# Kernel optimization log

Hardware: AMD Instinct MI355X
Metric: run time of the kernel (lower is better)

Reference implementation:

```python
import jax, jax.numpy as jnp
import numpy as np

HIDDEN = 4096
N_HEADS = 32
N_KV = 8
HEAD_DIM = 128
ROPE_THETA = 10000.0
B, S = 2, 2048


def _rope_neox(x, cos, sin):
    # x: [B,S,H,D]; cos/sin: [B,S,1,D/2]
    half = x.shape[-1] // 2
    x1, x2 = x[..., :half], x[..., half:]
    return jnp.concatenate([x1 * cos - x2 * sin, x2 * cos + x1 * sin], axis=-1)


def setup_inputs() -> dict:
    key = jax.random.key(0)
    k1, k2, k3 = jax.random.split(key, 3)
    hidden_states = jax.random.normal(k1, (B, S, HIDDEN), dtype=jnp.float32)
    positions = jnp.arange(B * S, dtype=jnp.int32).reshape(B, S)
    q_size = N_HEADS * HEAD_DIM
    kv_size = N_KV * HEAD_DIM
    w_qkv = jax.random.normal(k2, (HIDDEN, q_size + 2 * kv_size), dtype=jnp.float32) * (HIDDEN ** -0.5)
    w_o = jax.random.normal(k3, (q_size, HIDDEN), dtype=jnp.float32) * (q_size ** -0.5)
    return {"hidden_states": hidden_states, "positions": positions, "w_qkv": w_qkv, "w_o": w_o}


def reference(hidden_states, positions, w_qkv, w_o):
    q_size = N_HEADS * HEAD_DIM
    kv_size = N_KV * HEAD_DIM
    b, s, _ = hidden_states.shape

    qkv = hidden_states @ w_qkv  # [B,S,q+2kv]
    q = qkv[..., :q_size].reshape(b, s, N_HEADS, HEAD_DIM)
    k = qkv[..., q_size:q_size + kv_size].reshape(b, s, N_KV, HEAD_DIM)
    v = qkv[..., q_size + kv_size:].reshape(b, s, N_KV, HEAD_DIM)

    # RoPE (neox style, full rotary dim)
    inv_freq = 1.0 / (ROPE_THETA ** (jnp.arange(0, HEAD_DIM, 2, dtype=jnp.float32) / HEAD_DIM))
    ang = positions.astype(jnp.float32)[..., None] * inv_freq  # [B,S,D/2]
    cos = jnp.cos(ang)[:, :, None, :]
    sin = jnp.sin(ang)[:, :, None, :]
    q = _rope_neox(q, cos, sin)
    k = _rope_neox(k, cos, sin)

    # GQA: expand kv heads to match q heads
    rep = N_HEADS // N_KV
    k = jnp.repeat(k, rep, axis=2)  # [B,S,H,D]
    v = jnp.repeat(v, rep, axis=2)

    scale = HEAD_DIM ** -0.5
    scores = jnp.einsum('bqhd,bkhd->bhqk', q, k) * scale  # [B,H,S,S]
    causal = jnp.tril(jnp.ones((s, s), dtype=bool))
    scores = jnp.where(causal[None, None], scores, jnp.finfo(scores.dtype).min)
    probs = jax.nn.softmax(scores, axis=-1)
    attn = jnp.einsum('bhqk,bkhd->bqhd', probs, v).reshape(b, s, q_size)
    return attn @ w_o
```

## Files before the change

### kernel.cpp

```cpp
#include <hip/hip_runtime.h>
#include <hip/hip_bf16.h>
#include <stdint.h>
#include <stddef.h>

typedef unsigned short u16;
typedef __bf16 bf16x8 __attribute__((ext_vector_type(8)));
typedef float f32x4 __attribute__((ext_vector_type(4)));
typedef float f32x16 __attribute__((ext_vector_type(16)));
typedef unsigned u32x2 __attribute__((ext_vector_type(2)));

#define NH 32
#define NKV 8
#define HD 128
#define QKV_N 6144
#define SEQ 2048

__device__ __forceinline__ u16 f2b(float x) {
  union { float f; unsigned u; } v; v.f = x;
  unsigned r = v.u + 0x7FFF + ((v.u >> 16) & 1);
  return (u16)(r >> 16);
}
__device__ __forceinline__ float b2f(u16 b) {
  union { float f; unsigned u; } v; v.u = ((unsigned)b) << 16;
  return v.f;
}
__device__ __forceinline__ void gload16(const void* g, void* l) {
  __builtin_amdgcn_global_load_lds((const __attribute__((address_space(1))) unsigned int*)g,
                                   (__attribute__((address_space(3))) unsigned int*)l, 16, 0, 0);
}
__device__ __forceinline__ unsigned pk(float lo, float hi) {
  union { __bf16 h[2]; unsigned w; } u;
  u.h[0] = (__bf16)lo; u.h[1] = (__bf16)hi;
  return u.w;
}
__device__ __forceinline__ void plswap(unsigned& a, unsigned& b) {
  u32x2 r = __builtin_amdgcn_permlane32_swap(a, b, false, false);
  a = r.x; b = r.y;
}
__device__ __forceinline__ float pl_partner_max(float x) {
  unsigned u = __float_as_uint(x);
  u32x2 r = __builtin_amdgcn_permlane32_swap(u, u, false, false);
  return fmaxf(__uint_as_float(r.x), __uint_as_float(r.y));
}
__device__ __forceinline__ float pl_partner_sum(float x) {
  unsigned u = __float_as_uint(x);
  u32x2 r = __builtin_amdgcn_permlane32_swap(u, u, false, false);
  return __uint_as_float(r.x) + __uint_as_float(r.y);
}

__global__ void cast_f32_bf16(const float* __restrict__ in, u16* __restrict__ out, int n) {
  int i = (blockIdx.x * blockDim.x + threadIdx.x) * 4;
  if (i >= n) return;
  float4 v = *(const float4*)&in[i];
  ushort4 o;
  o.x = f2b(v.x); o.y = f2b(v.y); o.z = f2b(v.z); o.w = f2b(v.w);
  *(ushort4*)&out[i] = o;
}

__global__ void cast_transpose(const float* __restrict__ in, u16* __restrict__ out, int K, int N) {
  __shared__ float t[32][33];
  int n0 = blockIdx.x * 32, k0 = blockIdx.y * 32;
  int tx = threadIdx.x, ty = threadIdx.y;
#pragma unroll
  for (int i = 0; i < 4; ++i)
    t[ty + i * 8][tx] = in[(size_t)(k0 + ty + i * 8) * N + n0 + tx];
  __syncthreads();
#pragma unroll
  for (int i = 0; i < 4; ++i)
    out[(size_t)(n0 + ty + i * 8) * K + k0 + tx] = f2b(t[tx][ty + i * 8]);
}

__device__ __forceinline__ void storeC(float* C, size_t i, float v) { C[i] = v; }
__device__ __forceinline__ void storeC(u16* C, size_t i, float v) { C[i] = f2b(v); }

template <typename OutT>
__global__ __launch_bounds__(512, 2) void gemm256(const u16* __restrict__ A, const u16* __restrict__ Bt,
                                                  OutT* __restrict__ C, int M, int N, int K) {
  __shared__ __align__(16) u16 sA[2 * 256 * 64];
  __shared__ __align__(16) u16 sB[2 * 256 * 64];
  const int nbx = N >> 8;
  const int nwg = (M >> 8) * nbx;
  const int cpx = nwg >> 3;
  const int wg = ((int)blockIdx.x & 7) * cpx + ((int)blockIdx.x >> 3);
  const int row0 = (wg / nbx) << 8, col0 = (wg % nbx) << 8;
  const int tid = threadIdx.x, w = tid >> 6, lane = tid & 63;
  const int wm = w >> 2, wn = w & 3;
  const int lq = lane & 15, lh = lane >> 4, x7 = lq & 7;
  const int o0 = (lh ^ x7) << 3, o1 = ((4 + lh) ^ x7) << 3;
  const int sr7 = (tid >> 3) & 7;
  const int nt = K >> 6;

  auto stage = [&](const u16* __restrict__ src, u16* lbase, int rblk, int half, int t) {
#pragma unroll
    for (int c = 0; c < 2; ++c) {
      const int g = c * 512 + tid;
      const int r = g >> 3, gc = g & 7;
      gload16(src + (size_t)(rblk + half * 128 + r) * K + t * 64 + ((gc ^ sr7) << 3),
              lbase + (half * 1024 + c * 512 + (w << 6)) * 8);
    }
  };

  f32x4 acc[4][4][2] = {};

  stage(A, sA, row0, 0, 0);
  stage(Bt, sB, col0, 0, 0);
  stage(Bt, sB, col0, 1, 0);
  stage(A, sA, row0, 1, 0);
  stage(A, sA + 16384, row0, 0, 1);
  stage(Bt, sB + 16384, col0, 0, 1);
  asm volatile("s_waitcnt vmcnt(6)" ::: "memory");
  __builtin_amdgcn_s_barrier();

  for (int t = 0; t < nt; ++t) {
    const int cur = t & 1;
    u16* curA = sA + cur * 16384;
    u16* curB = sB + cur * 16384;
    u16* nxtA = sA + (cur ^ 1) * 16384;
    u16* nxtB = sB + (cur ^ 1) * 16384;

    bf16x8 af[4][2], bfr[2][2][2];
    {
      const u16* pa = curA + (wm * 64 + lq) * 64;
#pragma unroll
      for (int mi = 0; mi < 4; ++mi) {
        af[mi][0] = *(const bf16x8*)&pa[mi * 1024 + o0];
        af[mi][1] = *(const bf16x8*)&pa[mi * 1024 + o1];
      }
#pragma unroll
      for (int bh = 0; bh < 2; ++bh) {
        const u16* pb = curB + (bh * 128 + wn * 32 + lq) * 64;
#pragma unroll
        for (int ni = 0; ni < 2; ++ni) {
          bfr[bh][ni][0] = *(const bf16x8*)&pb[ni * 1024 + o0];
          bfr[bh][ni][1] = *(const bf16x8*)&pb[ni * 1024 + o1];
        }
      }
    }
    if (t + 1 < nt) {
      stage(Bt, nxtB, col0, 1, t + 1);
      stage(A, nxtA, row0, 1, t + 1);
    }
    __builtin_amdgcn_s_barrier();
    __builtin_amdgcn_s_setprio(1);
#pragma unroll
    for (int ks = 0; ks < 2; ++ks)
#pragma unroll
      for (int mi = 0; mi < 4; ++mi)
#pragma unroll
        for (int ni = 0; ni < 2; ++ni) {
          acc[0][mi][ni] = __builtin_amdgcn_mfma_f32_16x16x32_bf16(af[mi][ks], bfr[0][ni][ks], acc[0][mi][ni], 0, 0, 0);
          acc[1][mi][ni] = __builtin_amdgcn_mfma_f32_16x16x32_bf16(af[mi][ks], bfr[1][ni][ks], acc[1][mi][ni], 0, 0, 0);
        }
    __builtin_amdgcn_s_setprio(0);
    if (t < nt - 1) asm volatile("s_waitcnt vmcnt(8)" ::: "memory");
    else            asm volatile("s_waitcnt vmcnt(0)" ::: "memory");
    __builtin_amdgcn_s_barrier();

    {
      const u16* pa = curA + (128 + wm * 64 + lq) * 64;
#pragma unroll
      for (int mi = 0; mi < 4; ++mi) {
        af[mi][0] = *(const bf16x8*)&pa[mi * 1024 + o0];
        af[mi][1] = *(const bf16x8*)&pa[mi * 1024 + o1];
      }
    }
    if (t + 2 < nt) {
      stage(A, curA, row0, 0, t + 2);
      stage(Bt, curB, col0, 0, t + 2);
    }
    __builtin_amdgcn_s_barrier();
    __builtin_amdgcn_s_setprio(1);
#pragma unroll
    for (int ks = 0; ks < 2; ++ks)
#pragma unroll
      for (int mi = 0; mi < 4; ++mi)
#pragma unroll
        for (int ni = 0; ni < 2; ++ni) {
          acc[2][mi][ni] = __builtin_amdgcn_mfma_f32_16x16x32_bf16(af[mi][ks], bfr[0][ni][ks], acc[2][mi][ni], 0, 0, 0);
          acc[3][mi][ni] = __builtin_amdgcn_mfma_f32_16x16x32_bf16(af[mi][ks], bfr[1][ni][ks], acc[3][mi][ni], 0, 0, 0);
        }
    __builtin_amdgcn_s_setprio(0);
    if (t < nt - 2)       asm volatile("s_waitcnt vmcnt(6)" ::: "memory");
    else if (t == nt - 2) asm volatile("s_waitcnt vmcnt(2)" ::: "memory");
    __builtin_amdgcn_s_barrier();
  }

#pragma unroll
  for (int q = 0; q < 4; ++q) {
    const int ah = q >> 1, bh = q & 1;
#pragma unroll
    for (int mi = 0; mi < 4; ++mi)
#pragma unroll
      for (int ni = 0; ni < 2; ++ni)
#pragma unroll
        for (int j = 0; j < 4; ++j) {
          const int row = row0 + ah * 128 + wm * 64 + mi * 16 + lh * 4 + j;
          const int col = col0 + bh * 128 + wn * 32 + ni * 16 + lq;
          storeC(C, (size_t)row * N + col, acc[q][mi][ni][j]);
        }
  }
}

__global__ void rope_kernel(u16* __restrict__ qkv, const int* __restrict__ pos, float qscale) {
  __shared__ float cs[64], sn[64];
  const int row = blockIdx.x;
  const int tid = threadIdx.x;
  if (tid < 64) {
    float p = (float)pos[row];
    float inv = exp2f(-(float)tid * 0.20762050593046f);
    float a = p * inv;
    cs[tid] = cosf(a);
    sn[tid] = sinf(a);
  }
  __syncthreads();
  const size_t base = (size_t)row * QKV_N;
  for (int i = tid; i < 40 * 64; i += 256) {
    const int h = i >> 6, d = i & 63;
    const size_t o = base + h * 128 + d;
    float x1 = b2f(qkv[o]), x2 = b2f(qkv[o + 64]);
    float c = cs[d], s = sn[d];
    float o1 = x1 * c - x2 * s;
    float o2 = x2 * c + x1 * s;
    if (h < NH) { o1 *= qscale; o2 *= qscale; }
    qkv[o] = f2b(o1);
    qkv[o + 64] = f2b(o2);
  }
}

__global__ void v_transpose(const u16* __restrict__ qkv, u16* __restrict__ vt) {
  __shared__ u16 t[32][33];
  const int b = blockIdx.z >> 3, kvh = blockIdx.z & 7;
  const int s0 = blockIdx.x * 32, d0 = blockIdx.y * 32;
  const int tx = threadIdx.x, ty = threadIdx.y;
#pragma unroll
  for (int i = 0; i < 4; ++i)
    t[ty + i * 8][tx] = qkv[(size_t)(b * SEQ + s0 + ty + i * 8) * QKV_N + 5120 + kvh * 128 + d0 + tx];
  __syncthreads();
#pragma unroll
  for (int i = 0; i < 4; ++i)
    vt[(size_t)((b * NKV + kvh) * HD + d0 + ty + i * 8) * SEQ + s0 + tx] = t[tx][ty + i * 8];
}

__global__ __launch_bounds__(512, 2) void attn_kernel(const u16* __restrict__ qkv, const u16* __restrict__ vt,
                                                      u16* __restrict__ attn) {
  __shared__ __align__(16) u16 sK[2][64 * 128];
  __shared__ __align__(16) u16 sV[2][128 * 64];
  const int b = blockIdx.z, h = blockIdx.y;
  const int qt = (b == 0) ? blockIdx.x : 7 - blockIdx.x;
  const int kvh = h >> 2;
  const int qb = qt * 256;
  const int tid = threadIdx.x, w = tid >> 6, lane = tid & 63;
  const int lq = lane & 31, hi = lane >> 5, x7 = lane & 7;
  const int qw = qb + (w << 5);
  const int qa = qw + lq;
  const int nt = 4 * (qt + 1);

  auto stage = [&](int buf, int kt) {
    const int k0 = kt * 64;
#pragma unroll
    for (int c = 0; c < 2; ++c) {
      const int g = c * 512 + tid;
      const int r = g >> 4, gc = g & 15;
      const int gs = gc ^ (r & 7);
      gload16(qkv + (size_t)(b * SEQ + k0 + r) * QKV_N + 4096 + kvh * 128 + gs * 8,
              &sK[buf][(c * 512 + (w << 6)) * 8]);
    }
#pragma unroll
    for (int c = 0; c < 2; ++c) {
      const int g = c * 512 + tid;
      const int r = g >> 3, gc = g & 7;
      const int gs = gc ^ (r & 7);
      gload16(vt + (size_t)((b * NKV + kvh) * HD + r) * SEQ + k0 + gs * 8,
              &sV[buf][(c * 512 + (w << 6)) * 8]);
    }
  };

  stage(0, 0);
  bf16x8 qf[8];
#pragma unroll
  for (int ks = 0; ks < 8; ++ks)
    qf[ks] = *(const bf16x8*)&qkv[(size_t)(b * SEQ + qw + lq) * QKV_N + h * 128 + ks * 16 + 8 * hi];

  f32x16 o[4] = {};
  float mreg = -1e30f, lreg = 0.f;

  asm volatile("s_waitcnt vmcnt(0)" ::: "memory");
  __builtin_amdgcn_s_barrier();

  for (int kt = 0; kt < nt; ++kt) {
    const int cur = kt & 1;
    const int k0 = kt * 64;
    if (kt + 1 < nt) {
      stage(cur ^ 1, kt + 1);
      asm volatile("s_waitcnt vmcnt(4)" ::: "memory");
    } else {
      asm volatile("s_waitcnt vmcnt(0)" ::: "memory");
    }
    __builtin_amdgcn_s_barrier();

    if (k0 <= qw + 31) {
      const u16* sk = sK[cur];
      f32x16 st0 = {}, st1 = {};
      __builtin_amdgcn_s_setprio(1);
#pragma unroll
      for (int ks = 0; ks < 8; ++ks) {
        const int g = ((2 * ks + hi) ^ x7) * 8;
        bf16x8 kf0 = *(const bf16x8*)&sk[lq * 128 + g];
        bf16x8 kf1 = *(const bf16x8*)&sk[(32 + lq) * 128 + g];
        st0 = __builtin_amdgcn_mfma_f32_32x32x16_bf16(kf0, qf[ks], st0, 0, 0, 0);
        st1 = __builtin_amdgcn_mfma_f32_32x32x16_bf16(kf1, qf[ks], st1, 0, 0, 0);
      }
      __builtin_amdgcn_s_setprio(0);
      if (k0 + 63 > qw) {
#pragma unroll
        for (int r = 0; r < 16; ++r) {
          const int cr = (r & 3) + 8 * (r >> 2) + 4 * hi;
          st0[r] = (k0 + cr <= qa) ? st0[r] : -1e30f;
          st1[r] = (k0 + 32 + cr <= qa) ? st1[r] : -1e30f;
        }
      }
      float a8[8];
#pragma unroll
      for (int r = 0; r < 8; ++r)
        a8[r] = fmaxf(fmaxf(st0[r], st0[r + 8]), fmaxf(st1[r], st1[r + 8]));
#pragma unroll
      for (int s = 4; s; s >>= 1)
#pragma unroll
        for (int r = 0; r < s; ++r) a8[r] = fmaxf(a8[r], a8[r + s]);
      const float pm = pl_partner_max(a8[0]);
      if (!__all(pm <= mreg + 8.f)) {
        const float mn = fmaxf(mreg, pm);
        const float al = exp2f(mreg - mn);
        lreg *= al;
        mreg = mn;
#pragma unroll
        for (int r = 0; r < 16; ++r) {
          const int cr = (r & 3) + 8 * (r >> 2) + 4 * hi;
          const float ar = __shfl(al, cr, 64);
#pragma unroll
          for (int dn = 0; dn < 4; ++dn) o[dn][r] *= ar;
        }
      }
#pragma unroll
      for (int r = 0; r < 16; ++r) {
        st0[r] = exp2f(st0[r] - mreg);
        st1[r] = exp2f(st1[r] - mreg);
      }
      float s8[8];
#pragma unroll
      for (int r = 0; r < 8; ++r)
        s8[r] = (st0[r] + st0[r + 8]) + (st1[r] + st1[r + 8]);
#pragma unroll
      for (int s = 4; s; s >>= 1)
#pragma unroll
        for (int r = 0; r < s; ++r) s8[r] += s8[r + s];
      lreg += pl_partner_sum(s8[0]);
      union U8 { unsigned w[4]; bf16x8 v; };
      U8 pa[4];
#define PACKFRAG(F, P0, P1, P2, P3, P4, P5, P6, P7)                   \
      {                                                               \
        unsigned a0 = pk(P0, P1), a1 = pk(P2, P3);                    \
        unsigned b0 = pk(P4, P5), b1 = pk(P6, P7);                    \
        plswap(a0, b0); plswap(a1, b1);                               \
        pa[F].w[0] = a0; pa[F].w[1] = a1; pa[F].w[2] = b0; pa[F].w[3] = b1; \
      }
      PACKFRAG(0, st0[0], st0[1], st0[2], st0[3], st0[4], st0[5], st0[6], st0[7])
      PACKFRAG(1, st0[8], st0[9], st0[10], st0[11], st0[12], st0[13], st0[14], st0[15])
      PACKFRAG(2, st1[0], st1[1], st1[2], st1[3], st1[4], st1[5], st1[6], st1[7])
      PACKFRAG(3, st1[8], st1[9], st1[10], st1[11], st1[12], st1[13], st1[14], st1[15])
#undef PACKFRAG
      const u16* sv = sV[cur];
      __builtin_amdgcn_s_setprio(1);
#pragma unroll
      for (int dn = 0; dn < 4; ++dn) {
#pragma unroll
        for (int ks = 0; ks < 4; ++ks) {
          bf16x8 vf = *(const bf16x8*)&sv[(dn * 32 + lq) * 64 + (((2 * ks + hi) ^ x7)) * 8];
          o[dn] = __builtin_amdgcn_mfma_f32_32x32x16_bf16(pa[ks].v, vf, o[dn], 0, 0, 0);
        }
      }
      __builtin_amdgcn_s_setprio(0);
    }
    __builtin_amdgcn_s_barrier();
  }

  const float inv = 1.0f / lreg;
#pragma unroll
  for (int r = 0; r < 16; ++r) {
    const int cr = (r & 3) + 8 * (r >> 2) + 4 * hi;
    const float fr = __shfl(inv, cr, 64);
    const size_t row = (size_t)(b * SEQ + qw + cr);
#pragma unroll
    for (int dn = 0; dn < 4; ++dn)
      attn[row * 4096 + h * 128 + dn * 32 + lq] = f2b(o[dn][r] * fr);
  }
}

extern "C" void kernel_launch(void* const* d_in, const int* in_sizes, int n_in,
                              void* d_out, int out_size, void* d_ws, size_t ws_size,
                              hipStream_t stream) {
  const float* hs = (const float*)d_in[0];
  const int* pos = (const int*)d_in[1];
  const float* w_qkv = (const float*)d_in[2];
  const float* w_o = (const float*)d_in[3];
  float* out = (float*)d_out;
  char* ws = (char*)d_ws;

  u16* hid = (u16*)ws;
  u16* attnb = hid;
  u16* wT = (u16*)(ws + 33554432);
  u16* qkv = (u16*)(ws + 83886080);
  u16* vt = (u16*)(ws + 134217728);

  const float qscale = 0.12751744f;

  cast_f32_bf16<<<16384, 256, 0, stream>>>(hs, hid, 4096 * 4096);
  cast_transpose<<<dim3(192, 128), dim3(32, 8), 0, stream>>>(w_qkv, wT, 4096, QKV_N);
  gemm256<u16><<<384, 512, 0, stream>>>(hid, wT, qkv, 4096, QKV_N, 4096);
  rope_kernel<<<4096, 256, 0, stream>>>(qkv, pos, qscale);
  v_transpose<<<dim3(64, 4, 16), dim3(32, 8), 0, stream>>>(qkv, vt);
  cast_transpose<<<dim3(128, 128), dim3(32, 8), 0, stream>>>(w_o, wT, 4096, 4096);
  attn_kernel<<<dim3(8, 32, 2), 512, 0, stream>>>(qkv, vt, attnb);
  gemm256<float><<<256, 512, 0, stream>>>(attnb, wT, out, 4096, 4096, 4096);
}
```

Before: 538.9 us.

## Split GEMM main loop into four quadrant phases with finer-grained staging

Restructures the 256x256 bf16 GEMM main loop from two phases per K-tile into four, each computing one accumulator quadrant. Each phase reads only the B-half it needs from LDS and issues a single staged global load, with vmcnt waits retuned to match. The intent is to interleave global loads more evenly with MFMA work and hold fewer B-fragment registers at once. The cost is twice as many workgroup barriers per iteration, and the retuned wait counts must stay correct.

After: 545.5 us. About the same (+1.2%).

```diff
diff --git a/kernel.cpp b/kernel.cpp
--- a/kernel.cpp
+++ b/kernel.cpp
@@ -108,7 +108,7 @@
   stage(A, sA, row0, 1, 0);
   stage(A, sA + 16384, row0, 0, 1);
   stage(Bt, sB + 16384, col0, 0, 1);
-  asm volatile("s_waitcnt vmcnt(6)" ::: "memory");
+  asm volatile("s_waitcnt vmcnt(8)" ::: "memory");
   __builtin_amdgcn_s_barrier();
 
   for (int t = 0; t < nt; ++t) {
@@ -117,8 +117,8 @@
     u16* curB = sB + cur * 16384;
     u16* nxtA = sA + (cur ^ 1) * 16384;
     u16* nxtB = sB + (cur ^ 1) * 16384;
-
-    bf16x8 af[4][2], bfr[2][2][2];
+    bf16x8 af[4][2], bl[2][2], bh[2][2];
+
     {
       const u16* pa = curA + (wm * 64 + lq) * 64;
 #pragma unroll
@@ -126,20 +126,14 @@
         af[mi][0] = *(const bf16x8*)&pa[mi * 1024 + o0];
         af[mi][1] = *(const bf16x8*)&pa[mi * 1024 + o1];
       }
-#pragma unroll
-      for (int bh = 0; bh < 2; ++bh) {
-        const u16* pb = curB + (bh * 128 + wn * 32 + lq) * 64;
-#pragma unroll
-        for (int ni = 0; ni < 2; ++ni) {
-          bfr[bh][ni][0] = *(const bf16x8*)&pb[ni * 1024 + o0];
-          bfr[bh][ni][1] = *(const bf16x8*)&pb[ni * 1024 + o1];
-        }
-      }
-    }
-    if (t + 1 < nt) {
-      stage(Bt, nxtB, col0, 1, t + 1);
-      stage(A, nxtA, row0, 1, t + 1);
-    }
+      const u16* pb = curB + (wn * 32 + lq) * 64;
+#pragma unroll
+      for (int ni = 0; ni < 2; ++ni) {
+        bl[ni][0] = *(const bf16x8*)&pb[ni * 1024 + o0];
+        bl[ni][1] = *(const bf16x8*)&pb[ni * 1024 + o1];
+      }
+    }
+    if (t + 1 < nt) stage(Bt, nxtB, col0, 1, t + 1);
     __builtin_amdgcn_s_barrier();
     __builtin_amdgcn_s_setprio(1);
 #pragma unroll
@@ -147,13 +141,32 @@
 #pragma unroll
       for (int mi = 0; mi < 4; ++mi)
 #pragma unroll
-        for (int ni = 0; ni < 2; ++ni) {
-          acc[0][mi][ni] = __builtin_amdgcn_mfma_f32_16x16x32_bf16(af[mi][ks], bfr[0][ni][ks], acc[0][mi][ni], 0, 0, 0);
-          acc[1][mi][ni] = __builtin_amdgcn_mfma_f32_16x16x32_bf16(af[mi][ks], bfr[1][ni][ks], acc[1][mi][ni], 0, 0, 0);
-        }
+        for (int ni = 0; ni < 2; ++ni)
+          acc[0][mi][ni] = __builtin_amdgcn_mfma_f32_16x16x32_bf16(af[mi][ks], bl[ni][ks], acc[0][mi][ni], 0, 0, 0);
     __builtin_amdgcn_s_setprio(0);
-    if (t < nt - 1) asm volatile("s_waitcnt vmcnt(8)" ::: "memory");
+    if (t < nt - 1) asm volatile("s_waitcnt vmcnt(6)" ::: "memory");
     else            asm volatile("s_waitcnt vmcnt(0)" ::: "memory");
+    __builtin_amdgcn_s_barrier();
+
+    {
+      const u16* pb = curB + (128 + wn * 32 + lq) * 64;
+#pragma unroll
+      for (int ni = 0; ni < 2; ++ni) {
+        bh[ni][0] = *(const bf16x8*)&pb[ni * 1024 + o0];
+        bh[ni][1] = *(const bf16x8*)&pb[ni * 1024 + o1];
+      }
+    }
+    if (t + 1 < nt) stage(A, nxtA, row0, 1, t + 1);
+    __builtin_amdgcn_s_barrier();
+    __builtin_amdgcn_s_setprio(1);
+#pragma unroll
+    for (int ks = 0; ks < 2; ++ks)
+#pragma unroll
+      for (int mi = 0; mi < 4; ++mi)
+#pragma unroll
+        for (int ni = 0; ni < 2; ++ni)
+          acc[1][mi][ni] = __builtin_amdgcn_mfma_f32_16x16x32_bf16(af[mi][ks], bh[ni][ks], acc[1][mi][ni], 0, 0, 0);
+    __builtin_amdgcn_s_setprio(0);
     __builtin_amdgcn_s_barrier();
 
     {
@@ -164,10 +177,7 @@
         af[mi][1] = *(const bf16x8*)&pa[mi * 1024 + o1];
       }
     }
-    if (t + 2 < nt) {
-      stage(A, curA, row0, 0, t + 2);
-      stage(Bt, curB, col0, 0, t + 2);
-    }
+    if (t + 2 < nt) stage(A, curA, row0, 0, t + 2);
     __builtin_amdgcn_s_barrier();
     __builtin_amdgcn_s_setprio(1);
 #pragma unroll
@@ -175,19 +185,30 @@
 #pragma unroll
       for (int mi = 0; mi < 4; ++mi)
 #pragma unroll
-        for (int ni = 0; ni < 2; ++ni) {
-          acc[2][mi][ni] = __builtin_amdgcn_mfma_f32_16x16x32_bf16(af[mi][ks], bfr[0][ni][ks], acc[2][mi][ni], 0, 0, 0);
-          acc[3][mi][ni] = __builtin_amdgcn_mfma_f32_16x16x32_bf16(af[mi][ks], bfr[1][ni][ks], acc[3][mi][ni], 0, 0, 0);
-        }
+        for (int ni = 0; ni < 2; ++ni)
+          acc[2][mi][ni] = __builtin_amdgcn_mfma_f32_16x16x32_bf16(af[mi][ks], bl[ni][ks], acc[2][mi][ni], 0, 0, 0);
     __builtin_amdgcn_s_setprio(0);
-    if (t < nt - 2)       asm volatile("s_waitcnt vmcnt(6)" ::: "memory");
-    else if (t == nt - 2) asm volatile("s_waitcnt vmcnt(2)" ::: "memory");
+    __builtin_amdgcn_s_barrier();
+
+    if (t + 2 < nt) stage(Bt, curB, col0, 0, t + 2);
+    __builtin_amdgcn_s_barrier();
+    __builtin_amdgcn_s_setprio(1);
+#pragma unroll
+    for (int ks = 0; ks < 2; ++ks)
+#pragma unroll
+      for (int mi = 0; mi < 4; ++mi)
+#pragma unroll
+        for (int ni = 0; ni < 2; ++ni)
+          acc[3][mi][ni] = __builtin_amdgcn_mfma_f32_16x16x32_bf16(af[mi][ks], bh[ni][ks], acc[3][mi][ni], 0, 0, 0);
+    __builtin_amdgcn_s_setprio(0);
+    if (t < nt - 2)       asm volatile("s_waitcnt vmcnt(8)" ::: "memory");
+    else if (t == nt - 2) asm volatile("s_waitcnt vmcnt(4)" ::: "memory");
     __builtin_amdgcn_s_barrier();
   }
 
 #pragma unroll
   for (int q = 0; q < 4; ++q) {
-    const int ah = q >> 1, bh = q & 1;
+    const int ah = q >> 1, bh2 = q & 1;
 #pragma unroll
     for (int mi = 0; mi < 4; ++mi)
 #pragma unroll
@@ -195,7 +216,7 @@
 #pragma unroll
         for (int j = 0; j < 4; ++j) {
           const int row = row0 + ah * 128 + wm * 64 + mi * 16 + lh * 4 + j;
-          const int col = col0 + bh * 128 + wn * 32 + ni * 16 + lq;
+          const int col = col0 + bh2 * 128 + wn * 32 + ni * 16 + lq;
           storeC(C, (size_t)row * N + col, acc[q][mi][ni][j]);
         }
   }
```
